# Optimization experiments

Measured on AMD Instinct MI355X. Metric: run time of the kernel, lower is better.

## Reference

```python
import jax, jax.numpy as jnp
import numpy as np

CHAN = 128
IN_CHAN = 3
NB_OUT = 10
K = 2  # maxPoolKer


def affine_grid(theta, H, W):
    # theta: [C,2,3] -> grid [C,H,W,2], torch F.affine_grid align_corners=False
    xs = (2.0 * jnp.arange(W, dtype=jnp.float32) + 1.0) / W - 1.0
    ys = (2.0 * jnp.arange(H, dtype=jnp.float32) + 1.0) / H - 1.0
    gx, gy = jnp.meshgrid(xs, ys)  # [H,W]
    base = jnp.stack([gx, gy, jnp.ones_like(gx)], axis=-1)  # [H,W,3]
    return jnp.einsum('crk,hwk->chwr', theta, base)  # [...,0]=x, [...,1]=y


def grid_sample(img, grid):
    # img [M,H,W], grid [M,H,W,2]; bilinear, zeros padding, align_corners=False
    M, H, W = img.shape
    ix = ((grid[..., 0] + 1.0) * W - 1.0) * 0.5
    iy = ((grid[..., 1] + 1.0) * H - 1.0) * 0.5
    x0 = jnp.floor(ix)
    y0 = jnp.floor(iy)
    wx = ix - x0
    wy = iy - y0

    def tap(xi, yi):
        valid = (xi >= 0) & (xi <= W - 1) & (yi >= 0) & (yi <= H - 1)
        xc = jnp.clip(xi, 0, W - 1).astype(jnp.int32)
        yc = jnp.clip(yi, 0, H - 1).astype(jnp.int32)
        v = jax.vmap(lambda im, y, x: im[y, x])(img, yc, xc)
        return jnp.where(valid, v, 0.0)

    v00 = tap(x0, y0)
    v01 = tap(x0 + 1.0, y0)
    v10 = tap(x0, y0 + 1.0)
    v11 = tap(x0 + 1.0, y0 + 1.0)
    return (1.0 - wy) * ((1.0 - wx) * v00 + wx * v01) + wy * ((1.0 - wx) * v10 + wx * v11)


def geom_layer(x, geo, lin, box):
    # x [B,Ci,H,W]; lin [C,Ci]; geo,box [C,2,3]
    B, Ci, H, W = x.shape
    C = lin.shape[0]
    y = jnp.einsum('ci,bihw->bchw', lin, x)  # channel linear combine
    grid = affine_grid(geo, H, W)            # [C,H,W,2], shared across batch
    samp = jax.vmap(lambda yb: grid_sample(yb, grid))(y)  # [B,C,H,W]
    bgrid = affine_grid(box, H, W)
    boxm = grid_sample(jnp.ones((C, H, W), samp.dtype), bgrid)  # BoxPool mask
    return samp * boxm[None]


def maxpool_g(x, k):
    # MaxPool2d_G: depthwise box-filter conv -> argmax -> gather window from padded x
    B, C, H, W = x.shape
    ch, cw = H // k, W // k
    ker = jnp.ones((1, 1, ch, cw), x.dtype) / (ch + cw)
    xr = x.reshape(B * C, 1, H, W)
    conv = jax.lax.conv_general_dilated(
        xr, ker, (1, 1), [(ch // 2, ch // 2), (cw // 2, cw // 2)])
    conv = conv[:, :, :H, :W].reshape(B, C, H * W)
    argm = jnp.argmax(conv, axis=-1)
    r = argm // H  # original code uses origImgSize[0]; assumes square H==W
    c = argm % W
    padH, padW = H + H // k, W + W // k
    top = padH // 2 - H // 2
    left = padW // 2 - W // 2
    padded = jnp.zeros((B, C, padH, padW), x.dtype).at[:, :, top:top + H, left:left + W].set(x)
    r2 = r + H // (2 * k)
    c2 = c + W // (2 * k)
    ri = r2[..., None] + (jnp.arange(ch) - ch // 2)  # [B,C,ch]
    ci = c2[..., None] + (jnp.arange(cw) - cw // 2)  # [B,C,cw]
    gat = jax.vmap(jax.vmap(lambda p, rr, cc: p[rr[:, None], cc[None, :]]))(padded, ri, ci)
    return gat  # [B,C,ch,cw]


def setup_inputs() -> dict:
    key = jax.random.key(0)
    ks = jax.random.split(key, 12)
    eye = jnp.eye(3, dtype=jnp.float32)[:2]  # [2,3]
    x = jax.random.normal(ks[0], (8, IN_CHAN, 64, 64), dtype=jnp.float32)
    geo0 = eye[None] + 0.1 * jax.random.normal(ks[1], (CHAN, 2, 3), dtype=jnp.float32)
    lin0 = jax.random.uniform(ks[2], (CHAN, IN_CHAN), dtype=jnp.float32)
    box0 = eye[None] + 0.1 * jax.random.normal(ks[3], (CHAN, 2, 3), dtype=jnp.float32)
    geos = eye[None, None] + 0.1 * jax.random.normal(ks[4], (3, CHAN, 2, 3), dtype=jnp.float32)
    lins = jax.random.uniform(ks[5], (3, CHAN, CHAN), dtype=jnp.float32)
    boxes = eye[None, None] + 0.1 * jax.random.normal(ks[6], (3, CHAN, 2, 3), dtype=jnp.float32)
    bound = 1.0 / np.sqrt(CHAN)
    dense_w = jax.random.uniform(ks[7], (NB_OUT, CHAN), dtype=jnp.float32, minval=-bound, maxval=bound)
    dense_b = jax.random.uniform(ks[8], (NB_OUT,), dtype=jnp.float32, minval=-bound, maxval=bound)
    return {"x": x, "geo0": geo0, "lin0": lin0, "box0": box0,
            "geos": geos, "lins": lins, "boxes": boxes,
            "dense_w": dense_w, "dense_b": dense_b}


def reference(x, geo0, lin0, box0, geos, lins, boxes, dense_w, dense_b):
    h = geom_layer(x, geo0, lin0, box0)            # inLay: [8,128,64,64]
    h = geom_layer(h, geos[0], lins[0], boxes[0])  # layer 0
    h = maxpool_g(h, K)                            # layer 1 (maxPoolPos=1): [8,128,32,32]
    h = geom_layer(h, geos[1], lins[1], boxes[1])  # layer 2
    h = geom_layer(h, geos[2], lins[2], boxes[2])  # layer 3
    feat = h
    pooled = feat.mean(axis=-1).mean(axis=-1)      # [B,C]
    out = pooled @ dense_w.T + dense_b             # [B,nbOut]
    return out, feat
```

## Files before the change

kernel.cpp:

```cpp
#include <hip/hip_runtime.h>

#define BB 8
#define CC 128

__global__ __launch_bounds__(256) void inlay_sample_kernel(
    const float* __restrict__ x, const float* __restrict__ lin,
    const float* __restrict__ geo, const float* __restrict__ box,
    float* __restrict__ out) {
  const int H = 64, W = 64, HW = 4096;
  __shared__ __align__(16) float cp[64 * 68];
  int bc = blockIdx.x;
  int c = bc & (CC - 1);
  int b = bc >> 7;
  int tid = threadIdx.x;
  const float* xb = x + (size_t)b * 3 * HW;

  float w0 = lin[c * 3 + 0], w1 = lin[c * 3 + 1], w2 = lin[c * 3 + 2];

#pragma unroll
  for (int k = 0; k < 4; ++k) {
    int i4 = tid + k * 256;
    int base = i4 * 4;
    float4 f0 = *reinterpret_cast<const float4*>(&xb[base]);
    float4 f1 = *reinterpret_cast<const float4*>(&xb[HW + base]);
    float4 f2 = *reinterpret_cast<const float4*>(&xb[2 * HW + base]);
    float4 cv;
    cv.x = w0 * f0.x + w1 * f1.x + w2 * f2.x;
    cv.y = w0 * f0.y + w1 * f1.y + w2 * f2.y;
    cv.z = w0 * f0.z + w1 * f1.z + w2 * f2.z;
    cv.w = w0 * f0.w + w1 * f1.w + w2 * f2.w;
    int h = i4 >> 4, w = (i4 & 15) * 4;
    *reinterpret_cast<float4*>(&cp[h * 68 + w]) = cv;
  }
  __syncthreads();

  const float* g = geo + c * 6;
  const float* bx = box + c * 6;
  float g0 = g[0], g1 = g[1], g2 = g[2], g3 = g[3], g4 = g[4], g5 = g[5];
  float b0 = bx[0], b1 = bx[1], b2 = bx[2], b3 = bx[3], b4 = bx[4], b5 = bx[5];
  float* o = out + ((size_t)b * CC + c) * HW;

#pragma unroll
  for (int k = 0; k < 16; ++k) {
    int px = tid + k * 256;
    int h = px >> 6, w = px & 63;
    float xs = (2.0f * w + 1.0f) / W - 1.0f;
    float ys = (2.0f * h + 1.0f) / H - 1.0f;
    float gx = g0 * xs + g1 * ys + g2;
    float gy = g3 * xs + g4 * ys + g5;
    float ix = ((gx + 1.0f) * W - 1.0f) * 0.5f;
    float iy = ((gy + 1.0f) * H - 1.0f) * 0.5f;
    float x0 = floorf(ix), y0 = floorf(iy);
    float wx = ix - x0, wy = iy - y0;
    float v[2][2];
#pragma unroll
    for (int dy = 0; dy < 2; ++dy)
#pragma unroll
      for (int dx = 0; dx < 2; ++dx) {
        float xf = x0 + dx, yf = y0 + dy;
        bool valid = (xf >= 0.0f) && (xf <= 63.0f) && (yf >= 0.0f) && (yf <= 63.0f);
        int xi = (int)fminf(fmaxf(xf, 0.0f), 63.0f);
        int yi = (int)fminf(fmaxf(yf, 0.0f), 63.0f);
        v[dy][dx] = valid ? cp[yi * 68 + xi] : 0.0f;
      }
    float samp = (1.0f - wy) * ((1.0f - wx) * v[0][0] + wx * v[0][1]) +
                 wy * ((1.0f - wx) * v[1][0] + wx * v[1][1]);

    float bgx = b0 * xs + b1 * ys + b2;
    float bgy = b3 * xs + b4 * ys + b5;
    float bix = ((bgx + 1.0f) * W - 1.0f) * 0.5f;
    float biy = ((bgy + 1.0f) * H - 1.0f) * 0.5f;
    float bx0 = floorf(bix), by0 = floorf(biy);
    float bwx = bix - bx0, bwy = biy - by0;
    float m[2][2];
#pragma unroll
    for (int dy = 0; dy < 2; ++dy)
#pragma unroll
      for (int dx = 0; dx < 2; ++dx) {
        float xf = bx0 + dx, yf = by0 + dy;
        m[dy][dx] = ((xf >= 0.0f) && (xf <= 63.0f) && (yf >= 0.0f) && (yf <= 63.0f)) ? 1.0f : 0.0f;
      }
    float mask = (1.0f - bwy) * ((1.0f - bwx) * m[0][0] + bwx * m[0][1]) +
                 bwy * ((1.0f - bwx) * m[1][0] + bwx * m[1][1]);
    o[px] = samp * mask;
  }
}

__global__ __launch_bounds__(256) void gemm64_kernel(
    const float* __restrict__ lin, const float* __restrict__ x,
    float* __restrict__ y, int HW) {
  const int Ci = 128;
  __shared__ __align__(16) float As[16][68];
  __shared__ __align__(16) float Bs[16][64];
  int b = blockIdx.z;
  const float* xb = x + (size_t)b * Ci * HW;
  float* yb = y + (size_t)b * CC * HW;
  int tid = threadIdx.x;
  int tx = tid & 15, ty = tid >> 4;
  int row0 = blockIdx.y * 64;
  int col0 = blockIdx.x * 64;
  int m = tid >> 2, kq = (tid & 3) * 4;
  int kk = tid >> 4, n4 = (tid & 15) * 4;
  float acc[4][4] = {};
  float4 ra = *reinterpret_cast<const float4*>(&lin[(row0 + m) * Ci + kq]);
  float4 rb = *reinterpret_cast<const float4*>(&xb[(size_t)kk * HW + col0 + n4]);
  for (int k0 = 0; k0 < 128; k0 += 16) {
    __syncthreads();
    As[kq + 0][m] = ra.x; As[kq + 1][m] = ra.y; As[kq + 2][m] = ra.z; As[kq + 3][m] = ra.w;
    *reinterpret_cast<float4*>(&Bs[kk][n4]) = rb;
    __syncthreads();
    if (k0 + 16 < 128) {
      ra = *reinterpret_cast<const float4*>(&lin[(row0 + m) * Ci + k0 + 16 + kq]);
      rb = *reinterpret_cast<const float4*>(&xb[(size_t)(k0 + 16 + kk) * HW + col0 + n4]);
    }
#pragma unroll
    for (int kki = 0; kki < 16; ++kki) {
      float4 a4 = *reinterpret_cast<const float4*>(&As[kki][ty * 4]);
      float4 b4 = *reinterpret_cast<const float4*>(&Bs[kki][tx * 4]);
      float a[4] = {a4.x, a4.y, a4.z, a4.w};
      float bv[4] = {b4.x, b4.y, b4.z, b4.w};
#pragma unroll
      for (int i = 0; i < 4; i++)
#pragma unroll
        for (int j = 0; j < 4; j++) acc[i][j] += a[i] * bv[j];
    }
  }
#pragma unroll
  for (int i = 0; i < 4; i++) {
    float* yr = yb + (size_t)(row0 + ty * 4 + i) * HW + col0 + tx * 4;
    *reinterpret_cast<float4*>(yr) = make_float4(acc[i][0], acc[i][1], acc[i][2], acc[i][3]);
  }
}

__global__ __launch_bounds__(1024, 4) void sampmax_kernel(
    const float* __restrict__ y, const float* __restrict__ geo,
    const float* __restrict__ box, float* __restrict__ out) {
  __shared__ __align__(16) float sp[64 * 68];
  __shared__ __align__(16) float arena[64 * 100];
  __shared__ float wv[16];
  __shared__ int wi[16];
  __shared__ int am_s;
  float* pl = arena;
  float* cb = arena;

  int bc = blockIdx.x;
  int c = bc & (CC - 1);
  int b = bc >> 7;
  int tid = threadIdx.x;

  const float* plane = y + (size_t)bc * 4096;
  *reinterpret_cast<float4*>(&pl[tid * 4]) = *reinterpret_cast<const float4*>(&plane[tid * 4]);
  __syncthreads();

  {
    const float* g = geo + c * 6;
    const float* bx = box + c * 6;
    float g0 = g[0], g1 = g[1], g2 = g[2], g3 = g[3], g4 = g[4], g5 = g[5];
    float b0 = bx[0], b1 = bx[1], b2 = bx[2], b3 = bx[3], b4 = bx[4], b5 = bx[5];
#pragma unroll
    for (int k = 0; k < 4; ++k) {
      int px = tid + k * 1024;
      int h = px >> 6, w = px & 63;
      float xs = (2.0f * w + 1.0f) / 64.0f - 1.0f;
      float ys = (2.0f * h + 1.0f) / 64.0f - 1.0f;
      float gx = g0 * xs + g1 * ys + g2;
      float gy = g3 * xs + g4 * ys + g5;
      float ix = ((gx + 1.0f) * 64.0f - 1.0f) * 0.5f;
      float iy = ((gy + 1.0f) * 64.0f - 1.0f) * 0.5f;
      float x0 = floorf(ix), y0 = floorf(iy);
      float wx = ix - x0, wy = iy - y0;
      float v[2][2];
#pragma unroll
      for (int dy = 0; dy < 2; ++dy)
#pragma unroll
        for (int dx = 0; dx < 2; ++dx) {
          float xf = x0 + dx, yf = y0 + dy;
          bool valid = (xf >= 0.0f) && (xf <= 63.0f) && (yf >= 0.0f) && (yf <= 63.0f);
          int xi = (int)fminf(fmaxf(xf, 0.0f), 63.0f);
          int yi = (int)fminf(fmaxf(yf, 0.0f), 63.0f);
          v[dy][dx] = valid ? pl[yi * 64 + xi] : 0.0f;
        }
      float samp = (1.0f - wy) * ((1.0f - wx) * v[0][0] + wx * v[0][1]) +
                   wy * ((1.0f - wx) * v[1][0] + wx * v[1][1]);
      float bgx = b0 * xs + b1 * ys + b2;
      float bgy = b3 * xs + b4 * ys + b5;
      float bix = ((bgx + 1.0f) * 64.0f - 1.0f) * 0.5f;
      float biy = ((bgy + 1.0f) * 64.0f - 1.0f) * 0.5f;
      float bx0 = floorf(bix), by0 = floorf(biy);
      float bwx = bix - bx0, bwy = biy - by0;
      float m[2][2];
#pragma unroll
      for (int dy = 0; dy < 2; ++dy)
#pragma unroll
        for (int dx = 0; dx < 2; ++dx) {
          float xf = bx0 + dx, yf = by0 + dy;
          m[dy][dx] = ((xf >= 0.0f) && (xf <= 63.0f) && (yf >= 0.0f) && (yf <= 63.0f)) ? 1.0f : 0.0f;
        }
      float mask = (1.0f - bwy) * ((1.0f - bwx) * m[0][0] + bwx * m[0][1]) +
                   bwy * ((1.0f - bwx) * m[1][0] + bwx * m[1][1]);
      sp[h * 68 + w] = samp * mask;
    }
  }
  __syncthreads();

  if (tid < 256) {
    int strip = tid >> 4, w4 = (tid & 15) * 4;
    int h0 = strip * 4;
    float4 a0 = make_float4(0.f, 0.f, 0.f, 0.f), a1 = a0, a2 = a0, a3 = a0;
#pragma unroll
    for (int j = 0; j < 35; ++j) {
      int r = h0 + j - 16;
      bool valid = (r >= 0) && (r < 64);
      int rc = valid ? r : 0;
      float4 f = *reinterpret_cast<const float4*>(&sp[rc * 68 + w4]);
      f.x = valid ? f.x : 0.0f; f.y = valid ? f.y : 0.0f;
      f.z = valid ? f.z : 0.0f; f.w = valid ? f.w : 0.0f;
      if (j <= 31) { a0.x += f.x; a0.y += f.y; a0.z += f.z; a0.w += f.w; }
      if (j >= 1 && j <= 32) { a1.x += f.x; a1.y += f.y; a1.z += f.z; a1.w += f.w; }
      if (j >= 2 && j <= 33) { a2.x += f.x; a2.y += f.y; a2.z += f.z; a2.w += f.w; }
      if (j >= 3) { a3.x += f.x; a3.y += f.y; a3.z += f.z; a3.w += f.w; }
    }
    *reinterpret_cast<float4*>(&cb[(h0 + 0) * 100 + 16 + w4]) = a0;
    *reinterpret_cast<float4*>(&cb[(h0 + 1) * 100 + 16 + w4]) = a1;
    *reinterpret_cast<float4*>(&cb[(h0 + 2) * 100 + 16 + w4]) = a2;
    *reinterpret_cast<float4*>(&cb[(h0 + 3) * 100 + 16 + w4]) = a3;
  } else if (tid < 768) {
    int l = tid - 256;
    int row = l >> 3, gq = l & 7;
    int base = row * 100 + ((gq < 4) ? gq * 4 : 80 + (gq - 4) * 4);
    *reinterpret_cast<float4*>(&cb[base]) = make_float4(0.f, 0.f, 0.f, 0.f);
  }
  __syncthreads();

  float best = -3.402823466e+38f;
  int bidx = 0x7fffffff;
  {
    int h = tid >> 4, w4 = (tid & 15) * 4;
    float s0 = 0.f, s1 = 0.f, s2 = 0.f, s3 = 0.f;
#pragma unroll
    for (int q = 0; q < 9; ++q) {
      float4 f = *reinterpret_cast<const float4*>(&cb[h * 100 + w4 + 4 * q]);
      float fe[4] = {f.x, f.y, f.z, f.w};
#pragma unroll
      for (int e = 0; e < 4; ++e) {
        int u = 4 * q + e;
        if (u <= 31) s0 += fe[e];
        if (u >= 1 && u <= 32) s1 += fe[e];
        if (u >= 2 && u <= 33) s2 += fe[e];
        if (u >= 3 && u <= 34) s3 += fe[e];
      }
    }
    float sv[4] = {s0, s1, s2, s3};
#pragma unroll
    for (int d = 0; d < 4; ++d) {
      int i = (h << 6) + w4 + d;
      if (sv[d] > best) { best = sv[d]; bidx = i; }
    }
  }
#pragma unroll
  for (int off = 32; off > 0; off >>= 1) {
    float v2 = __shfl_down(best, off);
    int i2 = __shfl_down(bidx, off);
    if (v2 > best || (v2 == best && i2 < bidx)) { best = v2; bidx = i2; }
  }
  if ((tid & 63) == 0) { wv[tid >> 6] = best; wi[tid >> 6] = bidx; }
  __syncthreads();
  if (tid == 0) {
    float bv = wv[0]; int bi = wi[0];
#pragma unroll
    for (int k = 1; k < 16; ++k)
      if (wv[k] > bv || (wv[k] == bv && wi[k] < bi)) { bv = wv[k]; bi = wi[k]; }
    am_s = bi;
  }
  __syncthreads();

  int am = am_s;
  int r = am >> 6, cx = am & 63;
  float* o = out + (size_t)bc * 1024;
  {
    int oi = tid >> 5, oj = tid & 31;
    int rr = r + oi - 16, cj = cx + oj - 16;
    bool v = (rr >= 0) && (rr < 64) && (cj >= 0) && (cj < 64);
    int rrc = v ? rr : 0, cjc = v ? cj : 0;
    o[tid] = v ? sp[rrc * 68 + cjc] : 0.0f;
  }
}

template <bool POOL>
__global__ __launch_bounds__(256) void fused32_kernel(
    const float* __restrict__ lin, const float* __restrict__ x,
    const float* __restrict__ geo, const float* __restrict__ box,
    float* __restrict__ out, float* __restrict__ pooled) {
  const int H = 32, W = 32, HW = 1024;
  __shared__ __align__(16) float pls[4][1024];
  __shared__ float wred[16];
  int b = blockIdx.x >> 5;
  int c0 = (blockIdx.x & 31) * 4;
  int tid = threadIdx.x;
  const float* xb = x + (size_t)b * 128 * HW;
  const float* l0 = lin + (c0 + 0) * 128;
  const float* l1 = lin + (c0 + 1) * 128;
  const float* l2 = lin + (c0 + 2) * 128;
  const float* l3 = lin + (c0 + 3) * 128;
  int px4 = tid * 4;

  float4 acc0 = make_float4(0.f, 0.f, 0.f, 0.f);
  float4 acc1 = acc0, acc2 = acc0, acc3 = acc0;
#pragma unroll 8
  for (int k = 0; k < 128; ++k) {
    float4 xv = *reinterpret_cast<const float4*>(&xb[(size_t)k * HW + px4]);
    float s0 = l0[k], s1 = l1[k], s2 = l2[k], s3 = l3[k];
    acc0.x += s0 * xv.x; acc0.y += s0 * xv.y; acc0.z += s0 * xv.z; acc0.w += s0 * xv.w;
    acc1.x += s1 * xv.x; acc1.y += s1 * xv.y; acc1.z += s1 * xv.z; acc1.w += s1 * xv.w;
    acc2.x += s2 * xv.x; acc2.y += s2 * xv.y; acc2.z += s2 * xv.z; acc2.w += s2 * xv.w;
    acc3.x += s3 * xv.x; acc3.y += s3 * xv.y; acc3.z += s3 * xv.z; acc3.w += s3 * xv.w;
  }
  *reinterpret_cast<float4*>(&pls[0][px4]) = acc0;
  *reinterpret_cast<float4*>(&pls[1][px4]) = acc1;
  *reinterpret_cast<float4*>(&pls[2][px4]) = acc2;
  *reinterpret_cast<float4*>(&pls[3][px4]) = acc3;
  __syncthreads();

  float psum[4] = {0.f, 0.f, 0.f, 0.f};
#pragma unroll
  for (int c = 0; c < 4; ++c) {
    const float* g = geo + (c0 + c) * 6;
    const float* bxp = box + (c0 + c) * 6;
    float g0 = g[0], g1 = g[1], g2 = g[2], g3 = g[3], g4 = g[4], g5 = g[5];
    float b0 = bxp[0], b1 = bxp[1], b2 = bxp[2], b3 = bxp[3], b4 = bxp[4], b5 = bxp[5];
    float* o = out + ((size_t)b * CC + c0 + c) * HW;
    const float* pl = pls[c];
#pragma unroll
    for (int k = 0; k < 4; ++k) {
      int px = tid + k * 256;
      int h = px >> 5, w = px & 31;
      float xs = (2.0f * w + 1.0f) / W - 1.0f;
      float ys = (2.0f * h + 1.0f) / H - 1.0f;
      float gx = g0 * xs + g1 * ys + g2;
      float gy = g3 * xs + g4 * ys + g5;
      float ix = ((gx + 1.0f) * W - 1.0f) * 0.5f;
      float iy = ((gy + 1.0f) * H - 1.0f) * 0.5f;
      float x0 = floorf(ix), y0 = floorf(iy);
      float wx = ix - x0, wy = iy - y0;
      float v[2][2];
#pragma unroll
      for (int dy = 0; dy < 2; ++dy)
#pragma unroll
        for (int dx = 0; dx < 2; ++dx) {
          float xf = x0 + dx, yf = y0 + dy;
          bool valid = (xf >= 0.0f) && (xf <= 31.0f) && (yf >= 0.0f) && (yf <= 31.0f);
          int xi = (int)fminf(fmaxf(xf, 0.0f), 31.0f);
          int yi = (int)fminf(fmaxf(yf, 0.0f), 31.0f);
          v[dy][dx] = valid ? pl[yi * 32 + xi] : 0.0f;
        }
      float samp = (1.0f - wy) * ((1.0f - wx) * v[0][0] + wx * v[0][1]) +
                   wy * ((1.0f - wx) * v[1][0] + wx * v[1][1]);
      float bgx = b0 * xs + b1 * ys + b2;
      float bgy = b3 * xs + b4 * ys + b5;
      float bix = ((bgx + 1.0f) * W - 1.0f) * 0.5f;
      float biy = ((bgy + 1.0f) * H - 1.0f) * 0.5f;
      float bx0 = floorf(bix), by0 = floorf(biy);
      float bwx = bix - bx0, bwy = biy - by0;
      float m[2][2];
#pragma unroll
      for (int dy = 0; dy < 2; ++dy)
#pragma unroll
        for (int dx = 0; dx < 2; ++dx) {
          float xf = bx0 + dx, yf = by0 + dy;
          m[dy][dx] = ((xf >= 0.0f) && (xf <= 31.0f) && (yf >= 0.0f) && (yf <= 31.0f)) ? 1.0f : 0.0f;
        }
      float mask = (1.0f - bwy) * ((1.0f - bwx) * m[0][0] + bwx * m[0][1]) +
                   bwy * ((1.0f - bwx) * m[1][0] + bwx * m[1][1]);
      float res = samp * mask;
      o[px] = res;
      if (POOL) psum[c] += res;
    }
  }
  if (POOL) {
    int lane = tid & 63, wid = tid >> 6;
#pragma unroll
    for (int c = 0; c < 4; ++c) {
      float r = psum[c];
#pragma unroll
      for (int off = 32; off > 0; off >>= 1) r += __shfl_down(r, off);
      if (lane == 0) wred[c * 4 + wid] = r;
    }
    __syncthreads();
    if (tid < 4) {
      float t = wred[tid * 4] + wred[tid * 4 + 1] + wred[tid * 4 + 2] + wred[tid * 4 + 3];
      pooled[b * CC + c0 + tid] = t * (1.0f / 1024.0f);
    }
  }
}

__global__ __launch_bounds__(128) void dense_kernel(
    const float* __restrict__ pooled, const float* __restrict__ w,
    const float* __restrict__ bias, float* __restrict__ out) {
  int t = threadIdx.x;
  if (t < 80) {
    int b = t / 10, o = t % 10;
    float s = bias[o];
    const float* pb = pooled + b * 128;
    const float* wo = w + o * 128;
    for (int c = 0; c < 128; ++c) s += pb[c] * wo[c];
    out[b * 10 + o] = s;
  }
}

extern "C" void kernel_launch(void* const* d_in, const int* in_sizes, int n_in,
                              void* d_out, int out_size, void* d_ws, size_t ws_size,
                              hipStream_t stream) {
  const float* x     = (const float*)d_in[0];
  const float* geo0  = (const float*)d_in[1];
  const float* lin0  = (const float*)d_in[2];
  const float* box0  = (const float*)d_in[3];
  const float* geos  = (const float*)d_in[4];
  const float* lins  = (const float*)d_in[5];
  const float* boxes = (const float*)d_in[6];
  const float* dw    = (const float*)d_in[7];
  const float* db    = (const float*)d_in[8];

  float* out  = (float*)d_out;
  float* feat = out + 80;
  float* ws   = (float*)d_ws;
  float* ws0  = ws;
  float* ws1  = ws + 4194304;
  float* pooled = ws + 8388608;

  inlay_sample_kernel<<<dim3(BB * CC), 256, 0, stream>>>(x, lin0, geo0, box0, ws1);
  gemm64_kernel<<<dim3(64, 2, BB), 256, 0, stream>>>(lins, ws1, ws0, 4096);
  sampmax_kernel<<<dim3(BB * CC), 1024, 0, stream>>>(ws0, geos, boxes, ws1);
  fused32_kernel<false><<<dim3(256), 256, 0, stream>>>(lins + 16384, ws1, geos + 768, boxes + 768, ws0, nullptr);
  fused32_kernel<true><<<dim3(256), 256, 0, stream>>>(lins + 32768, ws0, geos + 1536, boxes + 1536, feat, pooled);
  dense_kernel<<<1, 128, 0, stream>>>(pooled, dw, db, out);
}
```

Baseline: 169.3 us.

## Fuse layer-0 channel GEMM into sample+maxpool kernel, processing four channels per block

Replaces the separate tiled GEMM and the per-plane sample/maxpool kernel with one kernel. Each 1024-thread block computes four output channel planes of the channel-mixing product directly into shared memory, then runs grid-sample, box mask, box-filter argmax and window gather per channel. This removes the write and re-read of a full 64x64x128x8 intermediate through global memory and one launch. In exchange the GEMM becomes a register outer product that re-reads the input from global per block, only 256 blocks run, shared-memory use rises (four padded planes), and block index order is swapped to batch-minor for L2 reuse of the input.

Result: slower. 182.2 us (+7.6%).

```diff
diff --git a/kernel.cpp b/kernel.cpp
--- a/kernel.cpp
+++ b/kernel.cpp
@@ -86,80 +86,55 @@
   }
 }
 
-__global__ __launch_bounds__(256) void gemm64_kernel(
+__global__ __launch_bounds__(1024, 4) void fused_gs_kernel(
     const float* __restrict__ lin, const float* __restrict__ x,
-    float* __restrict__ y, int HW) {
-  const int Ci = 128;
-  __shared__ __align__(16) float As[16][68];
-  __shared__ __align__(16) float Bs[16][64];
-  int b = blockIdx.z;
-  const float* xb = x + (size_t)b * Ci * HW;
-  float* yb = y + (size_t)b * CC * HW;
-  int tid = threadIdx.x;
-  int tx = tid & 15, ty = tid >> 4;
-  int row0 = blockIdx.y * 64;
-  int col0 = blockIdx.x * 64;
-  int m = tid >> 2, kq = (tid & 3) * 4;
-  int kk = tid >> 4, n4 = (tid & 15) * 4;
-  float acc[4][4] = {};
-  float4 ra = *reinterpret_cast<const float4*>(&lin[(row0 + m) * Ci + kq]);
-  float4 rb = *reinterpret_cast<const float4*>(&xb[(size_t)kk * HW + col0 + n4]);
-  for (int k0 = 0; k0 < 128; k0 += 16) {
-    __syncthreads();
-    As[kq + 0][m] = ra.x; As[kq + 1][m] = ra.y; As[kq + 2][m] = ra.z; As[kq + 3][m] = ra.w;
-    *reinterpret_cast<float4*>(&Bs[kk][n4]) = rb;
-    __syncthreads();
-    if (k0 + 16 < 128) {
-      ra = *reinterpret_cast<const float4*>(&lin[(row0 + m) * Ci + k0 + 16 + kq]);
-      rb = *reinterpret_cast<const float4*>(&xb[(size_t)(k0 + 16 + kk) * HW + col0 + n4]);
-    }
-#pragma unroll
-    for (int kki = 0; kki < 16; ++kki) {
-      float4 a4 = *reinterpret_cast<const float4*>(&As[kki][ty * 4]);
-      float4 b4 = *reinterpret_cast<const float4*>(&Bs[kki][tx * 4]);
-      float a[4] = {a4.x, a4.y, a4.z, a4.w};
-      float bv[4] = {b4.x, b4.y, b4.z, b4.w};
-#pragma unroll
-      for (int i = 0; i < 4; i++)
-#pragma unroll
-        for (int j = 0; j < 4; j++) acc[i][j] += a[i] * bv[j];
-    }
-  }
-#pragma unroll
-  for (int i = 0; i < 4; i++) {
-    float* yr = yb + (size_t)(row0 + ty * 4 + i) * HW + col0 + tx * 4;
-    *reinterpret_cast<float4*>(yr) = make_float4(acc[i][0], acc[i][1], acc[i][2], acc[i][3]);
-  }
-}
-
-__global__ __launch_bounds__(1024, 4) void sampmax_kernel(
-    const float* __restrict__ y, const float* __restrict__ geo,
-    const float* __restrict__ box, float* __restrict__ out) {
+    const float* __restrict__ geo, const float* __restrict__ box,
+    float* __restrict__ out) {
+  __shared__ __align__(16) float planes[4][64 * 68];
   __shared__ __align__(16) float sp[64 * 68];
-  __shared__ __align__(16) float arena[64 * 100];
+  __shared__ __align__(16) float cb[64 * 100];
   __shared__ float wv[16];
   __shared__ int wi[16];
   __shared__ int am_s;
-  float* pl = arena;
-  float* cb = arena;
-
-  int bc = blockIdx.x;
-  int c = bc & (CC - 1);
-  int b = bc >> 7;
+
+  int b = blockIdx.x & 7;
+  int c0 = (blockIdx.x >> 3) * 4;
   int tid = threadIdx.x;
-
-  const float* plane = y + (size_t)bc * 4096;
-  *reinterpret_cast<float4*>(&pl[tid * 4]) = *reinterpret_cast<const float4*>(&plane[tid * 4]);
+  const float* xb = x + (size_t)b * 128 * 4096;
+  const float* l0 = lin + (c0 + 0) * 128;
+  const float* l1 = lin + (c0 + 1) * 128;
+  const float* l2 = lin + (c0 + 2) * 128;
+  const float* l3 = lin + (c0 + 3) * 128;
+  int px4 = tid * 4;
+  int ph = tid >> 4, pw4 = (tid & 15) * 4;
+
+  float4 a0 = make_float4(0.f, 0.f, 0.f, 0.f);
+  float4 a1 = a0, a2 = a0, a3 = a0;
+#pragma unroll 8
+  for (int k = 0; k < 128; ++k) {
+    float4 xv = *reinterpret_cast<const float4*>(&xb[(size_t)k * 4096 + px4]);
+    float s0 = l0[k], s1 = l1[k], s2 = l2[k], s3 = l3[k];
+    a0.x += s0 * xv.x; a0.y += s0 * xv.y; a0.z += s0 * xv.z; a0.w += s0 * xv.w;
+    a1.x += s1 * xv.x; a1.y += s1 * xv.y; a1.z += s1 * xv.z; a1.w += s1 * xv.w;
+    a2.x += s2 * xv.x; a2.y += s2 * xv.y; a2.z += s2 * xv.z; a2.w += s2 * xv.w;
+    a3.x += s3 * xv.x; a3.y += s3 * xv.y; a3.z += s3 * xv.z; a3.w += s3 * xv.w;
+  }
+  *reinterpret_cast<float4*>(&planes[0][ph * 68 + pw4]) = a0;
+  *reinterpret_cast<float4*>(&planes[1][ph * 68 + pw4]) = a1;
+  *reinterpret_cast<float4*>(&planes[2][ph * 68 + pw4]) = a2;
+  *reinterpret_cast<float4*>(&planes[3][ph * 68 + pw4]) = a3;
   __syncthreads();
 
-  {
-    const float* g = geo + c * 6;
-    const float* bx = box + c * 6;
+  for (int c = 0; c < 4; ++c) {
+    const float* g = geo + (c0 + c) * 6;
+    const float* bx = box + (c0 + c) * 6;
     float g0 = g[0], g1 = g[1], g2 = g[2], g3 = g[3], g4 = g[4], g5 = g[5];
     float b0 = bx[0], b1 = bx[1], b2 = bx[2], b3 = bx[3], b4 = bx[4], b5 = bx[5];
-#pragma unroll
-    for (int k = 0; k < 4; ++k) {
-      int px = tid + k * 1024;
+    const float* pl = planes[c];
+
+#pragma unroll
+    for (int kk = 0; kk < 4; ++kk) {
+      int px = tid + kk * 1024;
       int h = px >> 6, w = px & 63;
       float xs = (2.0f * w + 1.0f) / 64.0f - 1.0f;
       float ys = (2.0f * h + 1.0f) / 64.0f - 1.0f;
@@ -178,7 +153,7 @@
           bool valid = (xf >= 0.0f) && (xf <= 63.0f) && (yf >= 0.0f) && (yf <= 63.0f);
           int xi = (int)fminf(fmaxf(xf, 0.0f), 63.0f);
           int yi = (int)fminf(fmaxf(yf, 0.0f), 63.0f);
-          v[dy][dx] = valid ? pl[yi * 64 + xi] : 0.0f;
+          v[dy][dx] = valid ? pl[yi * 68 + xi] : 0.0f;
         }
       float samp = (1.0f - wy) * ((1.0f - wx) * v[0][0] + wx * v[0][1]) +
                    wy * ((1.0f - wx) * v[1][0] + wx * v[1][1]);
@@ -200,89 +175,90 @@
                    bwy * ((1.0f - bwx) * m[1][0] + bwx * m[1][1]);
       sp[h * 68 + w] = samp * mask;
     }
-  }
-  __syncthreads();
-
-  if (tid < 256) {
-    int strip = tid >> 4, w4 = (tid & 15) * 4;
-    int h0 = strip * 4;
-    float4 a0 = make_float4(0.f, 0.f, 0.f, 0.f), a1 = a0, a2 = a0, a3 = a0;
-#pragma unroll
-    for (int j = 0; j < 35; ++j) {
-      int r = h0 + j - 16;
-      bool valid = (r >= 0) && (r < 64);
-      int rc = valid ? r : 0;
-      float4 f = *reinterpret_cast<const float4*>(&sp[rc * 68 + w4]);
-      f.x = valid ? f.x : 0.0f; f.y = valid ? f.y : 0.0f;
-      f.z = valid ? f.z : 0.0f; f.w = valid ? f.w : 0.0f;
-      if (j <= 31) { a0.x += f.x; a0.y += f.y; a0.z += f.z; a0.w += f.w; }
-      if (j >= 1 && j <= 32) { a1.x += f.x; a1.y += f.y; a1.z += f.z; a1.w += f.w; }
-      if (j >= 2 && j <= 33) { a2.x += f.x; a2.y += f.y; a2.z += f.z; a2.w += f.w; }
-      if (j >= 3) { a3.x += f.x; a3.y += f.y; a3.z += f.z; a3.w += f.w; }
-    }
-    *reinterpret_cast<float4*>(&cb[(h0 + 0) * 100 + 16 + w4]) = a0;
-    *reinterpret_cast<float4*>(&cb[(h0 + 1) * 100 + 16 + w4]) = a1;
-    *reinterpret_cast<float4*>(&cb[(h0 + 2) * 100 + 16 + w4]) = a2;
-    *reinterpret_cast<float4*>(&cb[(h0 + 3) * 100 + 16 + w4]) = a3;
-  } else if (tid < 768) {
-    int l = tid - 256;
-    int row = l >> 3, gq = l & 7;
-    int base = row * 100 + ((gq < 4) ? gq * 4 : 80 + (gq - 4) * 4);
-    *reinterpret_cast<float4*>(&cb[base]) = make_float4(0.f, 0.f, 0.f, 0.f);
-  }
-  __syncthreads();
-
-  float best = -3.402823466e+38f;
-  int bidx = 0x7fffffff;
-  {
-    int h = tid >> 4, w4 = (tid & 15) * 4;
-    float s0 = 0.f, s1 = 0.f, s2 = 0.f, s3 = 0.f;
-#pragma unroll
-    for (int q = 0; q < 9; ++q) {
-      float4 f = *reinterpret_cast<const float4*>(&cb[h * 100 + w4 + 4 * q]);
-      float fe[4] = {f.x, f.y, f.z, f.w};
-#pragma unroll
-      for (int e = 0; e < 4; ++e) {
-        int u = 4 * q + e;
-        if (u <= 31) s0 += fe[e];
-        if (u >= 1 && u <= 32) s1 += fe[e];
-        if (u >= 2 && u <= 33) s2 += fe[e];
-        if (u >= 3 && u <= 34) s3 += fe[e];
+    __syncthreads();
+
+    if (tid < 256) {
+      int strip = tid >> 4, w4 = (tid & 15) * 4;
+      int h0 = strip * 4;
+      float4 s0v = make_float4(0.f, 0.f, 0.f, 0.f), s1v = s0v, s2v = s0v, s3v = s0v;
+#pragma unroll
+      for (int j = 0; j < 35; ++j) {
+        int r = h0 + j - 16;
+        bool valid = (r >= 0) && (r < 64);
+        int rc = valid ? r : 0;
+        float4 f = *reinterpret_cast<const float4*>(&sp[rc * 68 + w4]);
+        f.x = valid ? f.x : 0.0f; f.y = valid ? f.y : 0.0f;
+        f.z = valid ? f.z : 0.0f; f.w = valid ? f.w : 0.0f;
+        if (j <= 31) { s0v.x += f.x; s0v.y += f.y; s0v.z += f.z; s0v.w += f.w; }
+        if (j >= 1 && j <= 32) { s1v.x += f.x; s1v.y += f.y; s1v.z += f.z; s1v.w += f.w; }
+        if (j >= 2 && j <= 33) { s2v.x += f.x; s2v.y += f.y; s2v.z += f.z; s2v.w += f.w; }
+        if (j >= 3) { s3v.x += f.x; s3v.y += f.y; s3v.z += f.z; s3v.w += f.w; }
       }
-    }
-    float sv[4] = {s0, s1, s2, s3};
-#pragma unroll
-    for (int d = 0; d < 4; ++d) {
-      int i = (h << 6) + w4 + d;
-      if (sv[d] > best) { best = sv[d]; bidx = i; }
-    }
-  }
-#pragma unroll
-  for (int off = 32; off > 0; off >>= 1) {
-    float v2 = __shfl_down(best, off);
-    int i2 = __shfl_down(bidx, off);
-    if (v2 > best || (v2 == best && i2 < bidx)) { best = v2; bidx = i2; }
-  }
-  if ((tid & 63) == 0) { wv[tid >> 6] = best; wi[tid >> 6] = bidx; }
-  __syncthreads();
-  if (tid == 0) {
-    float bv = wv[0]; int bi = wi[0];
-#pragma unroll
-    for (int k = 1; k < 16; ++k)
-      if (wv[k] > bv || (wv[k] == bv && wi[k] < bi)) { bv = wv[k]; bi = wi[k]; }
-    am_s = bi;
-  }
-  __syncthreads();
-
-  int am = am_s;
-  int r = am >> 6, cx = am & 63;
-  float* o = out + (size_t)bc * 1024;
-  {
-    int oi = tid >> 5, oj = tid & 31;
-    int rr = r + oi - 16, cj = cx + oj - 16;
-    bool v = (rr >= 0) && (rr < 64) && (cj >= 0) && (cj < 64);
-    int rrc = v ? rr : 0, cjc = v ? cj : 0;
-    o[tid] = v ? sp[rrc * 68 + cjc] : 0.0f;
+      *reinterpret_cast<float4*>(&cb[(h0 + 0) * 100 + 16 + w4]) = s0v;
+      *reinterpret_cast<float4*>(&cb[(h0 + 1) * 100 + 16 + w4]) = s1v;
+      *reinterpret_cast<float4*>(&cb[(h0 + 2) * 100 + 16 + w4]) = s2v;
+      *reinterpret_cast<float4*>(&cb[(h0 + 3) * 100 + 16 + w4]) = s3v;
+    } else if (tid < 768) {
+      int l = tid - 256;
+      int row = l >> 3, gq = l & 7;
+      int base = row * 100 + ((gq < 4) ? gq * 4 : 80 + (gq - 4) * 4);
+      *reinterpret_cast<float4*>(&cb[base]) = make_float4(0.f, 0.f, 0.f, 0.f);
+    }
+    __syncthreads();
+
+    float best = -3.402823466e+38f;
+    int bidx = 0x7fffffff;
+    {
+      int h = tid >> 4, w4 = (tid & 15) * 4;
+      float s0 = 0.f, s1 = 0.f, s2 = 0.f, s3 = 0.f;
+#pragma unroll
+      for (int q = 0; q < 9; ++q) {
+        float4 f = *reinterpret_cast<const float4*>(&cb[h * 100 + w4 + 4 * q]);
+        float fe[4] = {f.x, f.y, f.z, f.w};
+#pragma unroll
+        for (int e = 0; e < 4; ++e) {
+          int u = 4 * q + e;
+          if (u <= 31) s0 += fe[e];
+          if (u >= 1 && u <= 32) s1 += fe[e];
+          if (u >= 2 && u <= 33) s2 += fe[e];
+          if (u >= 3 && u <= 34) s3 += fe[e];
+        }
+      }
+      float sv[4] = {s0, s1, s2, s3};
+#pragma unroll
+      for (int d = 0; d < 4; ++d) {
+        int i = (h << 6) + w4 + d;
+        if (sv[d] > best) { best = sv[d]; bidx = i; }
+      }
+    }
+#pragma unroll
+    for (int off = 32; off > 0; off >>= 1) {
+      float v2 = __shfl_down(best, off);
+      int i2 = __shfl_down(bidx, off);
+      if (v2 > best || (v2 == best && i2 < bidx)) { best = v2; bidx = i2; }
+    }
+    if ((tid & 63) == 0) { wv[tid >> 6] = best; wi[tid >> 6] = bidx; }
+    __syncthreads();
+    if (tid == 0) {
+      float bv = wv[0]; int bi = wi[0];
+#pragma unroll
+      for (int k = 1; k < 16; ++k)
+        if (wv[k] > bv || (wv[k] == bv && wi[k] < bi)) { bv = wv[k]; bi = wi[k]; }
+      am_s = bi;
+    }
+    __syncthreads();
+
+    int am = am_s;
+    int r = am >> 6, cx = am & 63;
+    float* o = out + ((size_t)b * CC + c0 + c) * 1024;
+    {
+      int oi = tid >> 5, oj = tid & 31;
+      int rr = r + oi - 16, cj = cx + oj - 16;
+      bool v = (rr >= 0) && (rr < 64) && (cj >= 0) && (cj < 64);
+      int rrc = v ? rr : 0, cjc = v ? cj : 0;
+      o[tid] = v ? sp[rrc * 68 + cjc] : 0.0f;
+    }
+    __syncthreads();
   }
 }
 
@@ -294,8 +270,8 @@
   const int H = 32, W = 32, HW = 1024;
   __shared__ __align__(16) float pls[4][1024];
   __shared__ float wred[16];
-  int b = blockIdx.x >> 5;
-  int c0 = (blockIdx.x & 31) * 4;
+  int b = blockIdx.x & 7;
+  int c0 = (blockIdx.x >> 3) * 4;
   int tid = threadIdx.x;
   const float* xb = x + (size_t)b * 128 * HW;
   const float* l0 = lin + (c0 + 0) * 128;
@@ -428,9 +404,8 @@
   float* pooled = ws + 8388608;
 
   inlay_sample_kernel<<<dim3(BB * CC), 256, 0, stream>>>(x, lin0, geo0, box0, ws1);
-  gemm64_kernel<<<dim3(64, 2, BB), 256, 0, stream>>>(lins, ws1, ws0, 4096);
-  sampmax_kernel<<<dim3(BB * CC), 1024, 0, stream>>>(ws0, geos, boxes, ws1);
-  fused32_kernel<false><<<dim3(256), 256, 0, stream>>>(lins + 16384, ws1, geos + 768, boxes + 768, ws0, nullptr);
-  fused32_kernel<true><<<dim3(256), 256, 0, stream>>>(lins + 32768, ws0, geos + 1536, boxes + 1536, feat, pooled);
+  fused_gs_kernel<<<dim3(256), 1024, 0, stream>>>(lins, ws1, geos, boxes, ws0);
+  fused32_kernel<false><<<dim3(256), 256, 0, stream>>>(lins + 16384, ws0, geos + 768, boxes + 768, ws1, nullptr);
+  fused32_kernel<true><<<dim3(256), 256, 0, stream>>>(lins + 32768, ws1, geos + 1536, boxes + 1536, feat, pooled);
   dense_kernel<<<1, 128, 0, stream>>>(pooled, dw, db, out);
 }
```
